# Kernel tuning notes

Measured on AMD Instinct MI355X. Metric: run time of the kernel, lower is better.

The kernel has to match this reference:

```python
import jax, jax.numpy as jnp
import numpy as np

N = 100000   # nodes
E = 1600000  # edges per relation (avg in-degree 16)
D = 128      # gcn_hidden (in_feat == out_feat)
R = 2        # relations: forward_edge, backward_edge


def setup_inputs() -> dict:
    key = jax.random.key(0)
    ks = jax.random.split(key, 8)
    x = jax.random.normal(ks[0], (N, D), dtype=jnp.float32)
    src_fwd = jax.random.randint(ks[1], (E,), 0, N, dtype=jnp.int32)
    dst_fwd = jax.random.randint(ks[2], (E,), 0, N, dtype=jnp.int32)
    src_bwd = jax.random.randint(ks[3], (E,), 0, N, dtype=jnp.int32)
    dst_bwd = jax.random.randint(ks[4], (E,), 0, N, dtype=jnp.int32)
    # xavier_uniform with relu gain sqrt(2)
    gain = np.sqrt(2.0)
    lim_rel = gain * np.sqrt(6.0 / (D + D))
    rel_weight = jax.random.uniform(ks[5], (R, D, D), minval=-lim_rel, maxval=lim_rel, dtype=jnp.float32)
    loop_weight = jax.random.uniform(ks[6], (D, D), minval=-lim_rel, maxval=lim_rel, dtype=jnp.float32)
    h_bias = jnp.zeros((D,), dtype=jnp.float32)
    return {
        'x': x,
        'src_fwd': src_fwd, 'dst_fwd': dst_fwd,
        'src_bwd': src_bwd, 'dst_bwd': dst_bwd,
        'rel_weight': rel_weight, 'loop_weight': loop_weight, 'h_bias': h_bias,
    }


def _rel_conv(x, src, dst, W):
    # dgl GraphConv(norm='right', weight per relation): scatter-sum src feats to
    # dst, divide by clamped in-degree, then matmul W (in_feat == out_feat so
    # order of matmul vs aggregation is mathematically equivalent).
    msg = x[src]                                            # [E, D] gather
    agg = jax.ops.segment_sum(msg, dst, num_segments=N)     # [N, D] scatter-add
    deg = jax.ops.segment_sum(jnp.ones((src.shape[0],), x.dtype), dst, num_segments=N)
    agg = agg / jnp.clip(deg, 1.0)[:, None]                 # right norm, deg clamp(min=1)
    return agg @ W                                          # [N, D]


def reference(x, src_fwd, dst_fwd, src_bwd, dst_bwd, rel_weight, loop_weight, h_bias):
    h = _rel_conv(x, src_fwd, dst_fwd, rel_weight[0])
    h = h + _rel_conv(x, src_bwd, dst_bwd, rel_weight[1])   # HeteroGraphConv sums per-relation results
    h = h + x @ loop_weight                                 # self loop
    h = h + h_bias                                          # bias
    h = jax.nn.relu(h)                                      # activation
    return h                                                # dropout is identity in eval
```

## Files before the change

kernel.cpp:

```cpp
#include <hip/hip_runtime.h>
#include <hip/hip_bf16.h>


#define DFEAT 128
#define CH2 16384
#define NBMAX 1600
#define CAP 3328

typedef __attribute__((ext_vector_type(8))) short short8v;
typedef __attribute__((ext_vector_type(4))) float float4v;

__global__ void convert_kernel(const float4* __restrict__ x4,
                               ushort4* __restrict__ xb4, int n4) {
    int i = blockIdx.x * blockDim.x + threadIdx.x;
    if (i >= n4) return;
    float4 v = x4[i];
    ushort4 o;
    o.x = __hip_bfloat16_raw(__float2bfloat16(v.x)).x;
    o.y = __hip_bfloat16_raw(__float2bfloat16(v.y)).x;
    o.z = __hip_bfloat16_raw(__float2bfloat16(v.z)).x;
    o.w = __hip_bfloat16_raw(__float2bfloat16(v.w)).x;
    xb4[i] = o;
}

__global__ void pack_b_kernel(const float* __restrict__ wrel,
                              const float* __restrict__ wloop,
                              unsigned short* __restrict__ wb) {
    int t = blockIdx.x * blockDim.x + threadIdx.x;
    if (t >= 12 * 8 * 64) return;
    int lane = t & 63;
    int kbase = (t >> 9) * 32 + (lane >> 4) * 8;
    int col = (((t >> 6) & 7) << 4) + (lane & 15);
    unsigned short tmp[8];
#pragma unroll
    for (int j = 0; j < 8; ++j) {
        int k = kbase + j;
        float v = (k < 256) ? wrel[k * DFEAT + col] : wloop[(k - 256) * DFEAT + col];
        tmp[j] = __hip_bfloat16_raw(__float2bfloat16(v)).x;
    }
    *(ushort4*)(wb + t * 8)     = make_ushort4(tmp[0], tmp[1], tmp[2], tmp[3]);
    *(ushort4*)(wb + t * 8 + 4) = make_ushort4(tmp[4], tmp[5], tmp[6], tmp[7]);
}

__global__ void zero_kernel(int* __restrict__ p, int n) {
    int i = blockIdx.x * blockDim.x + threadIdx.x;
    if (i < n) p[i] = 0;
}

__global__ __launch_bounds__(256) void hist_kernel(
        const int* __restrict__ dst0, const int* __restrict__ dst1,
        int* __restrict__ ghist, int N, int E, int NB) {
    __shared__ int h[NBMAX];
    int tid = threadIdx.x;
    for (int i = tid; i < NBMAX; i += 256) h[i] = 0;
    __syncthreads();
    int lo = blockIdx.x * CH2, hi = min(2 * E, lo + CH2);
    for (int i = lo + tid; i < hi; i += 256) {
        int r = (i >= E) ? 1 : 0;
        int e = i - r * E;
        int t = r ? dst1[e] : dst0[e];
        atomicAdd(&h[(r * N + t) >> 7], 1);
    }
    __syncthreads();
    for (int b = tid; b < NB; b += 256) {
        int c = h[b];
        if (c) atomicAdd(&ghist[b], c);
    }
}

__global__ __launch_bounds__(256) void scan_kernel(const int* __restrict__ ghist,
                                                   int* __restrict__ S,
                                                   int* __restrict__ cursor,
                                                   int n, int total) {
    __shared__ int psum[256];
    int t = threadIdx.x;
    int cs = (n + 255) / 256;
    int s = 0;
    for (int j = 0; j < cs; ++j) {
        int idx = t * cs + j;
        if (idx < n) s += ghist[idx];
    }
    psum[t] = s; __syncthreads();
    for (int off = 1; off < 256; off <<= 1) {
        int add = (t >= off) ? psum[t - off] : 0;
        __syncthreads();
        psum[t] += add;
        __syncthreads();
    }
    int run = psum[t] - s;
    for (int j = 0; j < cs; ++j) {
        int idx = t * cs + j;
        if (idx < n) { S[idx] = run; cursor[idx] = run; run += ghist[idx]; }
    }
    if (t == 0) S[n] = total;
}

__global__ __launch_bounds__(256) void bin_kernel(
        const int* __restrict__ src0, const int* __restrict__ dst0,
        const int* __restrict__ src1, const int* __restrict__ dst1,
        int* __restrict__ cursor, unsigned* __restrict__ binned, int N, int E) {
    __shared__ int cnt[NBMAX];
    __shared__ int base[NBMAX];
    int tid = threadIdx.x;
    for (int i = tid; i < NBMAX; i += 256) cnt[i] = 0;
    __syncthreads();
    int lo = blockIdx.x * CH2, hi = min(2 * E, lo + CH2);
    for (int i = lo + tid; i < hi; i += 256) {
        int r = (i >= E) ? 1 : 0;
        int e = i - r * E;
        int t = r ? dst1[e] : dst0[e];
        atomicAdd(&cnt[(r * N + t) >> 7], 1);
    }
    __syncthreads();
    for (int b = tid; b < NBMAX; b += 256) {
        int c = cnt[b];
        if (c) base[b] = atomicAdd(&cursor[b], c);
    }
    __syncthreads();
    for (int i = lo + tid; i < hi; i += 256) {
        int r = (i >= E) ? 1 : 0;
        int e = i - r * E;
        int s = r ? src1[e] : src0[e];
        int t = r ? dst1[e] : dst0[e];
        int p = r * N + t;
        int slot = atomicAdd(&base[p >> 7], 1);
        binned[slot] = ((unsigned)(p & 127) << 17) | (unsigned)s;
    }
}

__global__ __launch_bounds__(256) void agg_kernel(
        const uint2* __restrict__ xb2,
        const unsigned* __restrict__ binned,
        const int* __restrict__ S,
        unsigned short* __restrict__ aggb, int M) {
    __shared__ unsigned ebuf[CAP];
    __shared__ int cnt[128], cur[128], rs[128], sh[128];
    int tid = threadIdx.x;
    int b = blockIdx.x;
    int estart = S[b], eend = S[b + 1];
    int total = eend - estart;
    int P0 = b << 7;
    int hw = tid >> 5, lane = tid & 31;

    if (total <= CAP) {
        if (tid < 128) cnt[tid] = 0;
        __syncthreads();
        for (int i = estart + tid; i < eend; i += 256)
            atomicAdd(&cnt[binned[i] >> 17], 1);
        __syncthreads();
        if (tid < 128) sh[tid] = cnt[tid];
        __syncthreads();
        for (int off = 1; off < 128; off <<= 1) {
            int add = (tid < 128 && tid >= off) ? sh[tid - off] : 0;
            __syncthreads();
            if (tid < 128) sh[tid] += add;
            __syncthreads();
        }
        if (tid < 128) { rs[tid] = sh[tid] - cnt[tid]; cur[tid] = sh[tid] - cnt[tid]; }
        __syncthreads();
        for (int i = estart + tid; i < eend; i += 256) {
            unsigned v = binned[i];
            int slot = atomicAdd(&cur[v >> 17], 1);
            ebuf[slot] = v;
        }
        __syncthreads();

        for (int pi = 0; pi < 16; ++pi) {
            int pl = hw * 16 + pi;
            int s0 = rs[pl], c = cnt[pl];
            float a0 = 0.f, a1 = 0.f, a2 = 0.f, a3 = 0.f;
            int e = 0;
            for (; e + 4 <= c; e += 4) {
                int sA = ebuf[s0 + e] & 0x1FFFF;
                int sB = ebuf[s0 + e + 1] & 0x1FFFF;
                int sC = ebuf[s0 + e + 2] & 0x1FFFF;
                int sD = ebuf[s0 + e + 3] & 0x1FFFF;
                uint2 gA = xb2[(long long)sA * 32 + lane];
                uint2 gB = xb2[(long long)sB * 32 + lane];
                uint2 gC = xb2[(long long)sC * 32 + lane];
                uint2 gD = xb2[(long long)sD * 32 + lane];
                a0 += __uint_as_float(gA.x << 16) + __uint_as_float(gB.x << 16)
                    + __uint_as_float(gC.x << 16) + __uint_as_float(gD.x << 16);
                a1 += __uint_as_float(gA.x & 0xffff0000u) + __uint_as_float(gB.x & 0xffff0000u)
                    + __uint_as_float(gC.x & 0xffff0000u) + __uint_as_float(gD.x & 0xffff0000u);
                a2 += __uint_as_float(gA.y << 16) + __uint_as_float(gB.y << 16)
                    + __uint_as_float(gC.y << 16) + __uint_as_float(gD.y << 16);
                a3 += __uint_as_float(gA.y & 0xffff0000u) + __uint_as_float(gB.y & 0xffff0000u)
                    + __uint_as_float(gC.y & 0xffff0000u) + __uint_as_float(gD.y & 0xffff0000u);
            }
            for (; e < c; ++e) {
                int s = ebuf[s0 + e] & 0x1FFFF;
                uint2 g = xb2[(long long)s * 32 + lane];
                a0 += __uint_as_float(g.x << 16);
                a1 += __uint_as_float(g.x & 0xffff0000u);
                a2 += __uint_as_float(g.y << 16);
                a3 += __uint_as_float(g.y & 0xffff0000u);
            }
            int pg = P0 + pl;
            if (pg < M) {
                float inv = 1.0f / (float)max(c, 1);
                ushort4 w;
                w.x = __hip_bfloat16_raw(__float2bfloat16(a0 * inv)).x;
                w.y = __hip_bfloat16_raw(__float2bfloat16(a1 * inv)).x;
                w.z = __hip_bfloat16_raw(__float2bfloat16(a2 * inv)).x;
                w.w = __hip_bfloat16_raw(__float2bfloat16(a3 * inv)).x;
                *(ushort4*)(aggb + (long long)pg * DFEAT + 4 * lane) = w;
            }
        }
    } else {
        for (int pi = 0; pi < 16; ++pi) {
            int pl = hw * 16 + pi;
            float a0 = 0.f, a1 = 0.f, a2 = 0.f, a3 = 0.f;
            int c = 0;
            for (int i = estart; i < eend; ++i) {
                unsigned v = binned[i];
                if ((int)(v >> 17) == pl) {
                    ++c;
                    uint2 g = xb2[(long long)(v & 0x1FFFF) * 32 + lane];
                    a0 += __uint_as_float(g.x << 16);
                    a1 += __uint_as_float(g.x & 0xffff0000u);
                    a2 += __uint_as_float(g.y << 16);
                    a3 += __uint_as_float(g.y & 0xffff0000u);
                }
            }
            int pg = P0 + pl;
            if (pg < M) {
                float inv = 1.0f / (float)max(c, 1);
                ushort4 w;
                w.x = __hip_bfloat16_raw(__float2bfloat16(a0 * inv)).x;
                w.y = __hip_bfloat16_raw(__float2bfloat16(a1 * inv)).x;
                w.z = __hip_bfloat16_raw(__float2bfloat16(a2 * inv)).x;
                w.w = __hip_bfloat16_raw(__float2bfloat16(a3 * inv)).x;
                *(ushort4*)(aggb + (long long)pg * DFEAT + 4 * lane) = w;
            }
        }
    }
}

__global__ __launch_bounds__(256) void mfma_gemm_kernel(
        const unsigned short* __restrict__ aggb,
        const unsigned short* __restrict__ xb,
        const unsigned short* __restrict__ wb,
        const float* __restrict__ bias,
        float* __restrict__ out, int N) {
    int tid = threadIdx.x;
    int wv = tid >> 6, lane = tid & 63;
    int R0 = blockIdx.x * 128 + wv * 32;
    int mrow = lane & 15, quad = lane >> 4;

    float4v acc[2][8];
#pragma unroll
    for (int rt = 0; rt < 2; ++rt)
#pragma unroll
        for (int ct = 0; ct < 8; ++ct) acc[rt][ct] = (float4v){0.f, 0.f, 0.f, 0.f};

    int n0 = min(R0 + mrow, N - 1);
    int n1 = min(R0 + 16 + mrow, N - 1);

#pragma unroll
    for (int kc = 0; kc < 12; ++kc) {
        int off = (kc & 3) * 32 + quad * 8;
        const unsigned short* s0;
        const unsigned short* s1;
        if (kc < 4)      { s0 = aggb + (size_t)n0 * DFEAT;       s1 = aggb + (size_t)n1 * DFEAT; }
        else if (kc < 8) { s0 = aggb + (size_t)(N + n0) * DFEAT; s1 = aggb + (size_t)(N + n1) * DFEAT; }
        else             { s0 = xb + (size_t)n0 * DFEAT;         s1 = xb + (size_t)n1 * DFEAT; }
        short8v a0 = *(const short8v*)(s0 + off);
        short8v a1 = *(const short8v*)(s1 + off);
#pragma unroll
        for (int ct = 0; ct < 8; ++ct) {
            short8v bfr = *(const short8v*)(wb + (((kc * 8 + ct) << 6) + lane) * 8);
            acc[0][ct] = __builtin_amdgcn_mfma_f32_16x16x32_bf16(a0, bfr, acc[0][ct], 0, 0, 0);
            acc[1][ct] = __builtin_amdgcn_mfma_f32_16x16x32_bf16(a1, bfr, acc[1][ct], 0, 0, 0);
        }
    }

#pragma unroll
    for (int ct = 0; ct < 8; ++ct) {
        int col = ct * 16 + mrow;
        float bv = bias[col];
#pragma unroll
        for (int rt = 0; rt < 2; ++rt) {
#pragma unroll
            for (int i = 0; i < 4; ++i) {
                int row = R0 + rt * 16 + quad * 4 + i;
                if (row < N)
                    out[(size_t)row * DFEAT + col] = fmaxf(acc[rt][ct][i] + bv, 0.f);
            }
        }
    }
}

extern "C" void kernel_launch(void* const* d_in, const int* in_sizes, int n_in,
                              void* d_out, int out_size, void* d_ws, size_t ws_size,
                              hipStream_t stream) {
    const float* x      = (const float*)d_in[0];
    const int* src_fwd  = (const int*)d_in[1];
    const int* dst_fwd  = (const int*)d_in[2];
    const int* src_bwd  = (const int*)d_in[3];
    const int* dst_bwd  = (const int*)d_in[4];
    const float* wrel   = (const float*)d_in[5];
    const float* wloop  = (const float*)d_in[6];
    const float* hbias  = (const float*)d_in[7];
    float* out          = (float*)d_out;

    int N = in_sizes[0] / DFEAT;
    int E = in_sizes[1];
    int M = 2 * N;
    int TE = 2 * E;
    int NB = (M + 127) / 128;

    unsigned short* wb   = (unsigned short*)d_ws;
    unsigned* binned     = (unsigned*)(wb + 12 * 8 * 64 * 8);
    unsigned short* xb   = (unsigned short*)(binned + (size_t)TE);
    unsigned short* aggb = xb + (size_t)N * DFEAT;
    int* ghist           = (int*)(aggb + (size_t)M * DFEAT);
    int* S               = ghist + NB;
    int* cursor          = S + NB + 1;

    int n4 = N * (DFEAT / 4);
    convert_kernel<<<(n4 + 255) / 256, 256, 0, stream>>>(
        (const float4*)x, (ushort4*)xb, n4);

    pack_b_kernel<<<24, 256, 0, stream>>>(wrel, wloop, wb);

    zero_kernel<<<(NB + 255) / 256, 256, 0, stream>>>(ghist, NB);

    int nblk = (TE + CH2 - 1) / CH2;
    hist_kernel<<<nblk, 256, 0, stream>>>(dst_fwd, dst_bwd, ghist, N, E, NB);

    scan_kernel<<<1, 256, 0, stream>>>(ghist, S, cursor, NB, TE);

    bin_kernel<<<nblk, 256, 0, stream>>>(
        src_fwd, dst_fwd, src_bwd, dst_bwd, cursor, binned, N, E);

    agg_kernel<<<NB, 256, 0, stream>>>((const uint2*)xb, binned, S, aggb, M);

    mfma_gemm_kernel<<<(N + 127) / 128, 256, 0, stream>>>(
        aggb, xb, wb, hbias, out, N);
}
```

Measured before the change: 402.2 us.

## Fuse convert with histogram, fold zeroing into weight pack, prefetch gathers in aggregation

```diff
diff --git a/kernel.cpp b/kernel.cpp
--- a/kernel.cpp
+++ b/kernel.cpp
@@ -5,28 +5,28 @@
 #define DFEAT 128
 #define CH2 16384
 #define NBMAX 1600
-#define CAP 3328
+#define CAPN 2816
 
 typedef __attribute__((ext_vector_type(8))) short short8v;
 typedef __attribute__((ext_vector_type(4))) float float4v;
-
-__global__ void convert_kernel(const float4* __restrict__ x4,
-                               ushort4* __restrict__ xb4, int n4) {
-    int i = blockIdx.x * blockDim.x + threadIdx.x;
-    if (i >= n4) return;
-    float4 v = x4[i];
-    ushort4 o;
-    o.x = __hip_bfloat16_raw(__float2bfloat16(v.x)).x;
-    o.y = __hip_bfloat16_raw(__float2bfloat16(v.y)).x;
-    o.z = __hip_bfloat16_raw(__float2bfloat16(v.z)).x;
-    o.w = __hip_bfloat16_raw(__float2bfloat16(v.w)).x;
-    xb4[i] = o;
+typedef __attribute__((ext_vector_type(2))) unsigned int uint2v;
+typedef __attribute__((ext_vector_type(4))) unsigned short ushort4v;
+
+__device__ __forceinline__ float4v bfexp(uint2v g) {
+    float4v v;
+    v[0] = __uint_as_float(g[0] << 16);
+    v[1] = __uint_as_float(g[0] & 0xffff0000u);
+    v[2] = __uint_as_float(g[1] << 16);
+    v[3] = __uint_as_float(g[1] & 0xffff0000u);
+    return v;
 }
 
 __global__ void pack_b_kernel(const float* __restrict__ wrel,
                               const float* __restrict__ wloop,
-                              unsigned short* __restrict__ wb) {
+                              unsigned short* __restrict__ wb,
+                              int* __restrict__ ghist, int NB) {
     int t = blockIdx.x * blockDim.x + threadIdx.x;
+    if (t < NB) ghist[t] = 0;
     if (t >= 12 * 8 * 64) return;
     int lane = t & 63;
     int kbase = (t >> 9) * 32 + (lane >> 4) * 8;
@@ -42,29 +42,38 @@
     *(ushort4*)(wb + t * 8 + 4) = make_ushort4(tmp[4], tmp[5], tmp[6], tmp[7]);
 }
 
-__global__ void zero_kernel(int* __restrict__ p, int n) {
-    int i = blockIdx.x * blockDim.x + threadIdx.x;
-    if (i < n) p[i] = 0;
-}
-
-__global__ __launch_bounds__(256) void hist_kernel(
+__global__ __launch_bounds__(256) void conv_hist_kernel(
+        const float4v* __restrict__ x4, ushort4v* __restrict__ xb4, int n4,
         const int* __restrict__ dst0, const int* __restrict__ dst1,
-        int* __restrict__ ghist, int N, int E, int NB) {
-    __shared__ int h[NBMAX];
-    int tid = threadIdx.x;
-    for (int i = tid; i < NBMAX; i += 256) h[i] = 0;
-    __syncthreads();
-    int lo = blockIdx.x * CH2, hi = min(2 * E, lo + CH2);
-    for (int i = lo + tid; i < hi; i += 256) {
-        int r = (i >= E) ? 1 : 0;
-        int e = i - r * E;
-        int t = r ? dst1[e] : dst0[e];
-        atomicAdd(&h[(r * N + t) >> 7], 1);
-    }
-    __syncthreads();
-    for (int b = tid; b < NB; b += 256) {
-        int c = h[b];
-        if (c) atomicAdd(&ghist[b], c);
+        int* __restrict__ ghist, int N, int E, int NB, int nhb) {
+    if ((int)blockIdx.x < nhb) {
+        __shared__ int h[NBMAX];
+        int tid = threadIdx.x;
+        for (int i = tid; i < NBMAX; i += 256) h[i] = 0;
+        __syncthreads();
+        int lo = blockIdx.x * CH2, hi = min(2 * E, lo + CH2);
+        for (int i = lo + tid; i < hi; i += 256) {
+            int r = (i >= E) ? 1 : 0;
+            int e = i - r * E;
+            int t = r ? dst1[e] : dst0[e];
+            atomicAdd(&h[(r * N + t) >> 7], 1);
+        }
+        __syncthreads();
+        for (int b = tid; b < NB; b += 256) {
+            int c = h[b];
+            if (c) atomicAdd(&ghist[b], c);
+        }
+    } else {
+        int i = ((int)blockIdx.x - nhb) * 256 + threadIdx.x;
+        if (i < n4) {
+            float4v v = __builtin_nontemporal_load(x4 + i);
+            ushort4v o;
+            o[0] = __hip_bfloat16_raw(__float2bfloat16(v[0])).x;
+            o[1] = __hip_bfloat16_raw(__float2bfloat16(v[1])).x;
+            o[2] = __hip_bfloat16_raw(__float2bfloat16(v[2])).x;
+            o[3] = __hip_bfloat16_raw(__float2bfloat16(v[3])).x;
+            xb4[i] = o;
+        }
     }
 }
 
@@ -129,11 +138,12 @@
 }
 
 __global__ __launch_bounds__(256) void agg_kernel(
-        const uint2* __restrict__ xb2,
+        const uint2v* __restrict__ xb2,
         const unsigned* __restrict__ binned,
         const int* __restrict__ S,
         unsigned short* __restrict__ aggb, int M) {
-    __shared__ unsigned ebuf[CAP];
+    __shared__ unsigned ebA[CAPN];
+    __shared__ unsigned ebB[CAPN];
     __shared__ int cnt[128], cur[128], rs[128], sh[128];
     int tid = threadIdx.x;
     int b = blockIdx.x;
@@ -142,11 +152,13 @@
     int P0 = b << 7;
     int hw = tid >> 5, lane = tid & 31;
 
-    if (total <= CAP) {
+    if (total <= CAPN) {
         if (tid < 128) cnt[tid] = 0;
-        __syncthreads();
-        for (int i = estart + tid; i < eend; i += 256)
-            atomicAdd(&cnt[binned[i] >> 17], 1);
+        for (int i = tid; i < total; i += 256)
+            ebA[i] = __builtin_nontemporal_load(binned + estart + i);
+        __syncthreads();
+        for (int i = tid; i < total; i += 256)
+            atomicAdd(&cnt[ebA[i] >> 17], 1);
         __syncthreads();
         if (tid < 128) sh[tid] = cnt[tid];
         __syncthreads();
@@ -158,80 +170,82 @@
         }
         if (tid < 128) { rs[tid] = sh[tid] - cnt[tid]; cur[tid] = sh[tid] - cnt[tid]; }
         __syncthreads();
-        for (int i = estart + tid; i < eend; i += 256) {
-            unsigned v = binned[i];
+        for (int i = tid; i < total; i += 256) {
+            unsigned v = ebA[i];
             int slot = atomicAdd(&cur[v >> 17], 1);
-            ebuf[slot] = v;
+            ebB[slot] = v;
         }
         __syncthreads();
 
         for (int pi = 0; pi < 16; ++pi) {
             int pl = hw * 16 + pi;
             int s0 = rs[pl], c = cnt[pl];
-            float a0 = 0.f, a1 = 0.f, a2 = 0.f, a3 = 0.f;
+            float4v a = (float4v){0.f, 0.f, 0.f, 0.f};
             int e = 0;
-            for (; e + 4 <= c; e += 4) {
-                int sA = ebuf[s0 + e] & 0x1FFFF;
-                int sB = ebuf[s0 + e + 1] & 0x1FFFF;
-                int sC = ebuf[s0 + e + 2] & 0x1FFFF;
-                int sD = ebuf[s0 + e + 3] & 0x1FFFF;
-                uint2 gA = xb2[(long long)sA * 32 + lane];
-                uint2 gB = xb2[(long long)sB * 32 + lane];
-                uint2 gC = xb2[(long long)sC * 32 + lane];
-                uint2 gD = xb2[(long long)sD * 32 + lane];
-                a0 += __uint_as_float(gA.x << 16) + __uint_as_float(gB.x << 16)
-                    + __uint_as_float(gC.x << 16) + __uint_as_float(gD.x << 16);
-                a1 += __uint_as_float(gA.x & 0xffff0000u) + __uint_as_float(gB.x & 0xffff0000u)
-                    + __uint_as_float(gC.x & 0xffff0000u) + __uint_as_float(gD.x & 0xffff0000u);
-                a2 += __uint_as_float(gA.y << 16) + __uint_as_float(gB.y << 16)
-                    + __uint_as_float(gC.y << 16) + __uint_as_float(gD.y << 16);
-                a3 += __uint_as_float(gA.y & 0xffff0000u) + __uint_as_float(gB.y & 0xffff0000u)
-                    + __uint_as_float(gC.y & 0xffff0000u) + __uint_as_float(gD.y & 0xffff0000u);
+            if (c >= 4) {
+                int sA = ebB[s0]     & 0x1FFFF;
+                int sB = ebB[s0 + 1] & 0x1FFFF;
+                int sC = ebB[s0 + 2] & 0x1FFFF;
+                int sD = ebB[s0 + 3] & 0x1FFFF;
+                uint2v cAq = xb2[(size_t)sA * 32 + lane];
+                uint2v cBq = xb2[(size_t)sB * 32 + lane];
+                uint2v cCq = xb2[(size_t)sC * 32 + lane];
+                uint2v cDq = xb2[(size_t)sD * 32 + lane];
+                for (e = 4; e + 4 <= c; e += 4) {
+                    int nA = ebB[s0 + e]     & 0x1FFFF;
+                    int nB = ebB[s0 + e + 1] & 0x1FFFF;
+                    int nC = ebB[s0 + e + 2] & 0x1FFFF;
+                    int nD = ebB[s0 + e + 3] & 0x1FFFF;
+                    uint2v gA = xb2[(size_t)nA * 32 + lane];
+                    uint2v gB = xb2[(size_t)nB * 32 + lane];
+                    uint2v gC = xb2[(size_t)nC * 32 + lane];
+                    uint2v gD = xb2[(size_t)nD * 32 + lane];
+                    float4v t0 = bfexp(cAq) + bfexp(cBq);
+                    float4v t1 = bfexp(cCq) + bfexp(cDq);
+                    a += t0 + t1;
+                    cAq = gA; cBq = gB; cCq = gC; cDq = gD;
+                }
+                float4v t0 = bfexp(cAq) + bfexp(cBq);
+                float4v t1 = bfexp(cCq) + bfexp(cDq);
+                a += t0 + t1;
             }
             for (; e < c; ++e) {
-                int s = ebuf[s0 + e] & 0x1FFFF;
-                uint2 g = xb2[(long long)s * 32 + lane];
-                a0 += __uint_as_float(g.x << 16);
-                a1 += __uint_as_float(g.x & 0xffff0000u);
-                a2 += __uint_as_float(g.y << 16);
-                a3 += __uint_as_float(g.y & 0xffff0000u);
+                int s = ebB[s0 + e] & 0x1FFFF;
+                a += bfexp(xb2[(size_t)s * 32 + lane]);
             }
             int pg = P0 + pl;
             if (pg < M) {
                 float inv = 1.0f / (float)max(c, 1);
-                ushort4 w;
-                w.x = __hip_bfloat16_raw(__float2bfloat16(a0 * inv)).x;
-                w.y = __hip_bfloat16_raw(__float2bfloat16(a1 * inv)).x;
-                w.z = __hip_bfloat16_raw(__float2bfloat16(a2 * inv)).x;
-                w.w = __hip_bfloat16_raw(__float2bfloat16(a3 * inv)).x;
-                *(ushort4*)(aggb + (long long)pg * DFEAT + 4 * lane) = w;
+                ushort4v w;
+                w[0] = __hip_bfloat16_raw(__float2bfloat16(a[0] * inv)).x;
+                w[1] = __hip_bfloat16_raw(__float2bfloat16(a[1] * inv)).x;
+                w[2] = __hip_bfloat16_raw(__float2bfloat16(a[2] * inv)).x;
+                w[3] = __hip_bfloat16_raw(__float2bfloat16(a[3] * inv)).x;
+                __builtin_nontemporal_store(
+                    w, (ushort4v*)(aggb + (size_t)pg * DFEAT + 4 * lane));
             }
         }
     } else {
         for (int pi = 0; pi < 16; ++pi) {
             int pl = hw * 16 + pi;
-            float a0 = 0.f, a1 = 0.f, a2 = 0.f, a3 = 0.f;
+            float4v a = (float4v){0.f, 0.f, 0.f, 0.f};
             int c = 0;
             for (int i = estart; i < eend; ++i) {
                 unsigned v = binned[i];
                 if ((int)(v >> 17) == pl) {
                     ++c;
-                    uint2 g = xb2[(long long)(v & 0x1FFFF) * 32 + lane];
-                    a0 += __uint_as_float(g.x << 16);
-                    a1 += __uint_as_float(g.x & 0xffff0000u);
-                    a2 += __uint_as_float(g.y << 16);
-                    a3 += __uint_as_float(g.y & 0xffff0000u);
+                    a += bfexp(xb2[(size_t)(v & 0x1FFFF) * 32 + lane]);
                 }
             }
             int pg = P0 + pl;
             if (pg < M) {
                 float inv = 1.0f / (float)max(c, 1);
-                ushort4 w;
-                w.x = __hip_bfloat16_raw(__float2bfloat16(a0 * inv)).x;
-                w.y = __hip_bfloat16_raw(__float2bfloat16(a1 * inv)).x;
-                w.z = __hip_bfloat16_raw(__float2bfloat16(a2 * inv)).x;
-                w.w = __hip_bfloat16_raw(__float2bfloat16(a3 * inv)).x;
-                *(ushort4*)(aggb + (long long)pg * DFEAT + 4 * lane) = w;
+                ushort4v w;
+                w[0] = __hip_bfloat16_raw(__float2bfloat16(a[0] * inv)).x;
+                w[1] = __hip_bfloat16_raw(__float2bfloat16(a[1] * inv)).x;
+                w[2] = __hip_bfloat16_raw(__float2bfloat16(a[2] * inv)).x;
+                w[3] = __hip_bfloat16_raw(__float2bfloat16(a[3] * inv)).x;
+                *(ushort4v*)(aggb + (size_t)pg * DFEAT + 4 * lane) = w;
             }
         }
     }
@@ -285,7 +299,8 @@
             for (int i = 0; i < 4; ++i) {
                 int row = R0 + rt * 16 + quad * 4 + i;
                 if (row < N)
-                    out[(size_t)row * DFEAT + col] = fmaxf(acc[rt][ct][i] + bv, 0.f);
+                    __builtin_nontemporal_store(fmaxf(acc[rt][ct][i] + bv, 0.f),
+                                                out + (size_t)row * DFEAT + col);
             }
         }
     }
@@ -319,22 +334,20 @@
     int* cursor          = S + NB + 1;
 
     int n4 = N * (DFEAT / 4);
-    convert_kernel<<<(n4 + 255) / 256, 256, 0, stream>>>(
-        (const float4*)x, (ushort4*)xb, n4);
-
-    pack_b_kernel<<<24, 256, 0, stream>>>(wrel, wloop, wb);
-
-    zero_kernel<<<(NB + 255) / 256, 256, 0, stream>>>(ghist, NB);
-
-    int nblk = (TE + CH2 - 1) / CH2;
-    hist_kernel<<<nblk, 256, 0, stream>>>(dst_fwd, dst_bwd, ghist, N, E, NB);
+    int nconv = (n4 + 255) / 256;
+    int nhb = (TE + CH2 - 1) / CH2;
+
+    pack_b_kernel<<<24, 256, 0, stream>>>(wrel, wloop, wb, ghist, NB);
+
+    conv_hist_kernel<<<nhb + nconv, 256, 0, stream>>>(
+        (const float4v*)x, (ushort4v*)xb, n4, dst_fwd, dst_bwd, ghist, N, E, NB, nhb);
 
     scan_kernel<<<1, 256, 0, stream>>>(ghist, S, cursor, NB, TE);
 
-    bin_kernel<<<nblk, 256, 0, stream>>>(
+    bin_kernel<<<nhb, 256, 0, stream>>>(
         src_fwd, dst_fwd, src_bwd, dst_bwd, cursor, binned, N, E);
 
-    agg_kernel<<<NB, 256, 0, stream>>>((const uint2*)xb, binned, S, aggb, M);
+    agg_kernel<<<NB, 256, 0, stream>>>((const uint2v*)xb, binned, S, aggb, M);
 
     mfma_gemm_kernel<<<(N + 127) / 128, 256, 0, stream>>>(
         aggb, xb, wb, hbias, out, N);
```

Measured after the change: 403.3 us. About the same (+0.3%).
